# Optimization experiments

Hardware: AMD Instinct MI355X
Metric: run time of the kernel (lower is better)

Reference implementation:

```python
import jax, jax.numpy as jnp
import numpy as np

B, IMG, TXT = 1, 2048, 256
D_MODEL = 2048
HEADS, HEAD_DIM = 16, 128
INNER = HEADS * HEAD_DIM
EPS = 1e-5
SCALE = HEAD_DIM ** -0.5


def _rmsnorm(x, w):
    # normalize over last dim (head_dim)
    return (x * jax.lax.rsqrt(jnp.mean(x * x, axis=-1, keepdims=True) + EPS)) * w


def _rope(x, cos, sin):
    # x: (B, S, H, D); cos/sin: (S, D) with pairwise-repeated freqs (interleaved convention)
    c = cos[None, :, None, :]
    s = sin[None, :, None, :]
    x1 = x[..., 0::2]
    x2 = x[..., 1::2]
    rot = jnp.stack([-x2, x1], axis=-1).reshape(x.shape)
    return x * c + rot * s


def setup_inputs() -> dict:
    key = jax.random.key(0)
    ks = jax.random.split(key, 12)
    sc_in = D_MODEL ** -0.5
    sc_inner = INNER ** -0.5
    inp = {
        'hidden_states': jax.random.normal(ks[0], (B, IMG, D_MODEL), jnp.float32),
        'encoder_hidden_states': jax.random.normal(ks[1], (B, TXT, D_MODEL), jnp.float32),
    }
    # RoPE tables over the joint (text + image) sequence, interleaved pair layout
    pos = jnp.arange(TXT + IMG, dtype=jnp.float32)
    inv = 1.0 / (10000.0 ** (jnp.arange(0, HEAD_DIM, 2, dtype=jnp.float32) / HEAD_DIM))
    freqs = pos[:, None] * inv[None, :]
    freqs = jnp.repeat(freqs, 2, axis=-1)  # (S, HEAD_DIM)
    inp['freqs_cos'] = jnp.cos(freqs)
    inp['freqs_sin'] = jnp.sin(freqs)
    # parameters (stored (in, out))
    inp['Wqkv'] = jax.random.normal(ks[2], (D_MODEL, 3 * INNER), jnp.float32) * sc_in
    inp['Wqkv_add'] = jax.random.normal(ks[3], (D_MODEL, 3 * INNER), jnp.float32) * sc_in
    inp['b_qkv_add'] = jax.random.normal(ks[4], (3 * INNER,), jnp.float32) * 0.01
    inp['norm_q_w'] = jnp.ones((HEAD_DIM,), jnp.float32)
    inp['norm_k_w'] = jnp.ones((HEAD_DIM,), jnp.float32)
    inp['norm_aq_w'] = jnp.ones((HEAD_DIM,), jnp.float32)
    inp['norm_ak_w'] = jnp.ones((HEAD_DIM,), jnp.float32)
    inp['Wout'] = jax.random.normal(ks[5], (INNER, D_MODEL), jnp.float32) * sc_inner
    inp['b_out'] = jax.random.normal(ks[6], (D_MODEL,), jnp.float32) * 0.01
    inp['Wadd_out'] = jax.random.normal(ks[7], (INNER, D_MODEL), jnp.float32) * sc_inner
    inp['b_add_out'] = jax.random.normal(ks[8], (D_MODEL,), jnp.float32) * 0.01
    return inp


def reference(hidden_states, encoder_hidden_states, freqs_cos, freqs_sin,
              Wqkv, Wqkv_add, b_qkv_add, norm_q_w, norm_k_w, norm_aq_w, norm_ak_w,
              Wout, b_out, Wadd_out, b_add_out):
    b, s_img, _ = hidden_states.shape
    s_txt = encoder_hidden_states.shape[1]

    # fused QKV projection (image stream), chunk q/k/v, unflatten heads
    qkv = hidden_states @ Wqkv  # (B, IMG, 3*INNER)
    q, k, v = jnp.split(qkv, 3, axis=-1)
    q = _rmsnorm(q.reshape(b, s_img, HEADS, HEAD_DIM), norm_q_w)
    k = _rmsnorm(k.reshape(b, s_img, HEADS, HEAD_DIM), norm_k_w)
    v = v.reshape(b, s_img, HEADS, HEAD_DIM)

    # fused QKV projection (text stream, with bias)
    eqkv = encoder_hidden_states @ Wqkv_add + b_qkv_add
    eq, ek, ev = jnp.split(eqkv, 3, axis=-1)
    eq = _rmsnorm(eq.reshape(b, s_txt, HEADS, HEAD_DIM), norm_aq_w)
    ek = _rmsnorm(ek.reshape(b, s_txt, HEADS, HEAD_DIM), norm_ak_w)
    ev = ev.reshape(b, s_txt, HEADS, HEAD_DIM)

    # joint [text; image] concatenation, then RoPE on joint Q/K
    jq = jnp.concatenate([eq, q], axis=1)
    jk = jnp.concatenate([ek, k], axis=1)
    jv = jnp.concatenate([ev, v], axis=1)
    jq = _rope(jq, freqs_cos, freqs_sin)
    jk = _rope(jk, freqs_cos, freqs_sin)

    # non-causal scaled dot-product attention, layout (B, S, H, D)
    scores = jnp.einsum('bqhd,bkhd->bhqk', jq, jk) * SCALE
    probs = jax.nn.softmax(scores, axis=-1)
    out = jnp.einsum('bhqk,bkhd->bqhd', probs, jv)  # (B, S_joint, H, D)
    out = out.reshape(b, s_txt + s_img, INNER)

    enc_out = out[:, :s_txt]
    img_out = out[:, s_txt:]
    img_out = img_out @ Wout + b_out
    enc_out = enc_out @ Wadd_out + b_add_out
    return (img_out, enc_out)
```

## Files before the change

kernel.cpp:

```cpp
#include <hip/hip_runtime.h>
#include <stdint.h>

#define HEADS 16
#define HD 128
#define S_TXT 256
#define S_IMG 2048
#define S_ALL 2304
#define DMODEL 2048
#define N_QKV 6144
#define INNER 2048
#define ATT_EPS 1e-5f
#define ATT_SCALE 0.08838834764831845f
#define LOG2E 1.4426950408889634f
#define MBOUND 16.5f
#define QT_N 18
#define TPS 36

typedef __attribute__((ext_vector_type(8))) __bf16 bf16x8;
typedef __attribute__((ext_vector_type(4))) float f32x4;
typedef __attribute__((ext_vector_type(4))) uint32_t u32x4;

__device__ __forceinline__ uint16_t f2bf(float f) {
  union { float f; uint32_t u; } v; v.f = f;
  uint32_t r = (v.u + 0x7FFF + ((v.u >> 16) & 1)) >> 16;
  return (uint16_t)r;
}
__device__ __forceinline__ float bf2f(uint16_t h) {
  union { float f; uint32_t u; } v; v.u = ((uint32_t)h) << 16;
  return v.f;
}
__device__ __forceinline__ float fexp2(float x) {
#if __has_builtin(__builtin_amdgcn_exp2f)
  return __builtin_amdgcn_exp2f(x);
#else
  return __expf(x * 0.69314718055994531f);
#endif
}

__device__ __forceinline__ void async_cp16(const void* g, void* l) {
  __builtin_amdgcn_global_load_lds(
      (const __attribute__((address_space(1))) void*)g,
      (__attribute__((address_space(3))) void*)l, 16, 0, 0);
}

__global__ __launch_bounds__(256) void k_cvt(const float* __restrict__ src,
                                             uint16_t* __restrict__ dst, int n4) {
  int i = blockIdx.x * 256 + threadIdx.x;
  int stride = gridDim.x * 256;
  for (; i < n4; i += stride) {
    float4 v = ((const float4*)src)[i];
    uint16_t o[4];
    o[0] = f2bf(v.x); o[1] = f2bf(v.y); o[2] = f2bf(v.z); o[3] = f2bf(v.w);
    ((uint2*)dst)[i] = *(const uint2*)o;
  }
}

__global__ __launch_bounds__(256) void k_cvt_t4(
    const float* __restrict__ s0, uint16_t* __restrict__ d0,
    const float* __restrict__ s1, uint16_t* __restrict__ d1,
    const float* __restrict__ s2, uint16_t* __restrict__ d2,
    const float* __restrict__ s3, uint16_t* __restrict__ d3) {
  __shared__ float t[64][68];
  int b = blockIdx.x;
  const float* src; uint16_t* dst; int R, C, tb;
  if (b < 3072)      { src = s0; dst = d0; R = DMODEL; C = N_QKV;  tb = b; }
  else if (b < 6144) { src = s1; dst = d1; R = DMODEL; C = N_QKV;  tb = b - 3072; }
  else if (b < 7168) { src = s2; dst = d2; R = INNER;  C = DMODEL; tb = b - 6144; }
  else               { src = s3; dst = d3; R = INNER;  C = DMODEL; tb = b - 7168; }
  int ntr = R >> 6;
  int tr = tb % ntr, tc = tb / ntr;
  int tid = threadIdx.x;
  int rr = tid >> 4, c4 = (tid & 15) * 4;
#pragma unroll
  for (int j = 0; j < 4; ++j) {
    int r = rr + j * 16;
    float4 v = *(const float4*)&src[(size_t)(tr * 64 + r) * C + tc * 64 + c4];
    *(float4*)&t[r][c4] = v;
  }
  __syncthreads();
  int cc = tid >> 4, r4 = (tid & 15) * 4;
#pragma unroll
  for (int j = 0; j < 4; ++j) {
    int c = cc + j * 16;
    uint16_t ov[4];
    ov[0] = f2bf(t[r4 + 0][c]); ov[1] = f2bf(t[r4 + 1][c]);
    ov[2] = f2bf(t[r4 + 2][c]); ov[3] = f2bf(t[r4 + 3][c]);
    *(uint2*)&dst[(size_t)(tc * 64 + c) * R + tr * 64 + r4] = *(const uint2*)ov;
  }
}

template <bool OUT_BF16>
__global__ __launch_bounds__(512, 1) void k_gemm2(
    const uint16_t* __restrict__ A0, const uint16_t* __restrict__ B0,
    const float* __restrict__ bias0, void* __restrict__ C0,
    const uint16_t* __restrict__ A1, const uint16_t* __restrict__ B1,
    const float* __restrict__ bias1, void* __restrict__ C1,
    int seg0_tiles, int N, int K) {
  __shared__ __align__(16) char lds[3 * 49152];
  int bn = blockIdx.x, bm = blockIdx.y;
  const uint16_t* A; const uint16_t* B; const float* bias; void* C; int mrow;
  if (bm < seg0_tiles) { A = A0; B = B0; bias = bias0; C = C0; mrow = bm * 256; }
  else { A = A1; B = B1; bias = bias1; C = C1; mrow = (bm - seg0_tiles) * 256; }
  int tid = threadIdx.x, lane = tid & 63, w = tid >> 6;
  int g = lane >> 4, li = lane & 15;
  int wm = w >> 1, wn = w & 1;
  const int NKI = K / 64;

  int rowin = lane >> 3;
  int csrc = (lane & 7) ^ rowin;

  auto stage = [&](int t, char* buf) {
    int kt = t * 64;
#pragma unroll
    for (int j = 0; j < 4; ++j) {
      int r = w * 4 + j;
      int tr = r * 8 + rowin;
      async_cp16(A + (size_t)(mrow + tr) * K + kt + 8 * csrc, buf + r * 1024);
    }
#pragma unroll
    for (int j = 0; j < 2; ++j) {
      int r = w * 2 + j;
      int tr = r * 8 + rowin;
      async_cp16(B + (size_t)(bn * 128 + tr) * K + kt + 8 * csrc, buf + 32768 + r * 1024);
    }
  };

  f32x4 acc[4][4] = {};

  stage(0, lds);
  stage(1, lds + 49152);
  asm volatile("s_waitcnt vmcnt(6)" ::: "memory");
  __builtin_amdgcn_s_barrier();
  asm volatile("" ::: "memory");

  int cbuf = 0, sbuf = 2;
  for (int t = 0; t < NKI; ++t) {
    const char* cur = lds + cbuf * 49152;
    if (t + 2 < NKI) stage(t + 2, lds + sbuf * 49152);

    bf16x8 af[2][4], bfv[2][4];
#pragma unroll
    for (int kk = 0; kk < 2; ++kk) {
#pragma unroll
      for (int mi = 0; mi < 4; ++mi) {
        int row = wm * 64 + mi * 16 + li;
        int ch = (kk * 4 + g) ^ (row & 7);
        af[kk][mi] = __builtin_bit_cast(bf16x8, *(const u32x4*)(cur + row * 128 + ch * 16));
      }
#pragma unroll
      for (int ni = 0; ni < 4; ++ni) {
        int row = wn * 64 + ni * 16 + li;
        int ch = (kk * 4 + g) ^ (row & 7);
        bfv[kk][ni] = __builtin_bit_cast(bf16x8, *(const u32x4*)(cur + 32768 + row * 128 + ch * 16));
      }
    }
    __builtin_amdgcn_s_setprio(1);
#pragma unroll
    for (int kk = 0; kk < 2; ++kk)
#pragma unroll
      for (int mi = 0; mi < 4; ++mi)
#pragma unroll
        for (int ni = 0; ni < 4; ++ni)
          acc[mi][ni] = __builtin_amdgcn_mfma_f32_16x16x32_bf16(af[kk][mi], bfv[kk][ni], acc[mi][ni], 0, 0, 0);
    __builtin_amdgcn_s_setprio(0);

    if (t + 1 < NKI) {
      if (t + 2 < NKI) asm volatile("s_waitcnt vmcnt(6)" ::: "memory");
      else             asm volatile("s_waitcnt vmcnt(0)" ::: "memory");
      __builtin_amdgcn_s_barrier();
      asm volatile("" ::: "memory");
    }
    cbuf = (cbuf + 1 == 3) ? 0 : cbuf + 1;
    sbuf = (sbuf + 1 == 3) ? 0 : sbuf + 1;
  }

#pragma unroll
  for (int mi = 0; mi < 4; ++mi) {
#pragma unroll
    for (int ni = 0; ni < 4; ++ni) {
      int col = bn * 128 + wn * 64 + ni * 16 + li;
      float bv = bias ? bias[col] : 0.0f;
#pragma unroll
      for (int i = 0; i < 4; ++i) {
        int r = mrow + wm * 64 + mi * 16 + 4 * g + i;
        float v = acc[mi][ni][i] + bv;
        if (OUT_BF16) ((uint16_t*)C)[(size_t)r * N + col] = f2bf(v);
        else          ((float*)C)[(size_t)r * N + col] = v;
      }
    }
  }
}

__global__ __launch_bounds__(256) void k_post(
    const uint16_t* __restrict__ qkv_img, const uint16_t* __restrict__ qkv_txt,
    const float* __restrict__ fcos, const float* __restrict__ fsin,
    const float* __restrict__ wq, const float* __restrict__ wk,
    const float* __restrict__ waq, const float* __restrict__ wak,
    uint16_t* __restrict__ Qo, uint16_t* __restrict__ Ko, uint16_t* __restrict__ VTo) {
  int s = blockIdx.x;
  const uint16_t* row = (s < S_TXT) ? qkv_txt + (size_t)s * N_QKV
                                    : qkv_img + (size_t)(s - S_TXT) * N_QKV;
  const float* wqp = (s < S_TXT) ? waq : wq;
  const float* wkp = (s < S_TXT) ? wak : wk;
  int tid = threadIdx.x, lane = tid & 63, w = tid >> 6;
  int h = w * 4 + (lane >> 4);
  int d0 = (lane & 15) * 8;
  float cs[8], sn[8];
#pragma unroll
  for (int j = 0; j < 8; ++j) {
    cs[j] = fcos[s * HD + d0 + j];
    sn[j] = fsin[s * HD + d0 + j];
  }
#pragma unroll
  for (int part = 0; part < 2; ++part) {
    const uint16_t* src = row + part * INNER + h * HD + d0;
    u32x4 raw = *(const u32x4*)src;
    const uint16_t* rp = (const uint16_t*)&raw;
    float x[8], ss = 0.f;
#pragma unroll
    for (int j = 0; j < 8; ++j) { x[j] = bf2f(rp[j]); ss += x[j] * x[j]; }
    ss += __shfl_xor(ss, 1); ss += __shfl_xor(ss, 2);
    ss += __shfl_xor(ss, 4); ss += __shfl_xor(ss, 8);
    float rn = rsqrtf(ss * (1.0f / HD) + ATT_EPS);
    const float* wp = part ? wkp : wqp;
#pragma unroll
    for (int j = 0; j < 8; ++j) x[j] = x[j] * rn * wp[d0 + j];
    float y[8];
#pragma unroll
    for (int j = 0; j < 8; j += 2) {
      y[j]     = x[j] * cs[j] - x[j + 1] * sn[j];
      y[j + 1] = x[j + 1] * cs[j + 1] + x[j] * sn[j + 1];
    }
    float sc = part ? 1.0f : (ATT_SCALE * LOG2E);
    uint16_t ov[8];
#pragma unroll
    for (int j = 0; j < 8; ++j) ov[j] = f2bf(y[j] * sc);
    uint16_t* dst = (part ? Ko : Qo) + ((size_t)h * S_ALL + s) * HD + d0;
    *(u32x4*)dst = *(const u32x4*)ov;
  }
  {
    u32x4 raw = *(const u32x4*)(row + 2 * INNER + h * HD + d0);
    const uint16_t* rp = (const uint16_t*)&raw;
#pragma unroll
    for (int j = 0; j < 8; ++j)
      VTo[((size_t)h * HD + d0 + j) * S_ALL + s] = rp[j];
  }
}

__global__ __launch_bounds__(256, 3) void k_attn(
    const uint16_t* __restrict__ Qg, const uint16_t* __restrict__ Kg,
    const uint16_t* __restrict__ VTg,
    float* __restrict__ part0, float* __restrict__ part1,
    float* __restrict__ lsumP) {
  __shared__ __align__(16) char Kt[2][8192];
  __shared__ __align__(16) char Vt[2][8192];
  __shared__ __align__(16) uint16_t Pl[4][32 * 40];

  int b0 = blockIdx.x;
  int bid = (b0 & 7) * 72 + (b0 >> 3);
  int h = bid / 36, r6 = bid % 36, sp = r6 / 18, qt = r6 % 18;
  int tid = threadIdx.x, lane = tid & 63, w = tid >> 6;
  int g = lane >> 4, li = lane & 15;

  const uint16_t* Kh = Kg + (size_t)h * S_ALL * HD;
  const uint16_t* Vh = VTg + (size_t)h * HD * S_ALL;
  float* po = (sp ? part1 : part0) + ((size_t)(h * QT_N + qt) * 128 + w * 32) * 128;

  int qbase = qt * 128 + w * 32;
  bf16x8 qf[2][4];
#pragma unroll
  for (int q2 = 0; q2 < 2; ++q2) {
    const uint16_t* qp = Qg + ((size_t)h * S_ALL + qbase + q2 * 16 + li) * HD;
#pragma unroll
    for (int kc = 0; kc < 4; ++kc)
      qf[q2][kc] = __builtin_bit_cast(bf16x8, *(const u32x4*)(qp + kc * 32 + g * 8));
  }
  f32x4 o[2][8] = {};
  float lsum[2] = {0.f, 0.f};

  auto stage = [&](int tk, int buf) {
#pragma unroll
    for (int j = 0; j < 2; ++j) {
      int cj = w * 128 + j * 64 + lane;
      int row = cj >> 4, c = (cj & 15) ^ (row & 15);
      async_cp16(Kh + (size_t)(tk * 32 + row) * HD + 8 * c, Kt[buf] + (w * 128 + j * 64) * 16);
    }
#pragma unroll
    for (int j = 0; j < 2; ++j) {
      int cj = w * 128 + j * 64 + lane;
      int row = cj >> 2, c = (cj & 3) ^ ((row >> 1) & 3);
      async_cp16(Vh + (size_t)row * S_ALL + tk * 32 + 8 * c, Vt[buf] + (w * 128 + j * 64) * 16);
    }
  };

  int t0 = sp * TPS;
  stage(t0, 0);
  asm volatile("s_waitcnt vmcnt(0)" ::: "memory");
  __builtin_amdgcn_s_barrier();
  asm volatile("" ::: "memory");

  for (int t = 0; t < TPS; ++t) {
    int cur = t & 1;
    if (t + 1 < TPS) stage(t0 + t + 1, cur ^ 1);
    const char* KtC = Kt[cur];
    const char* VtC = Vt[cur];

    f32x4 sc[2][2];
#pragma unroll
    for (int q2 = 0; q2 < 2; ++q2)
#pragma unroll
      for (int kb = 0; kb < 2; ++kb)
        sc[q2][kb] = (f32x4){-MBOUND, -MBOUND, -MBOUND, -MBOUND};
    __builtin_amdgcn_s_setprio(1);
#pragma unroll
    for (int kb = 0; kb < 2; ++kb)
#pragma unroll
      for (int kc = 0; kc < 4; ++kc) {
        int ch = (kc * 4 + g) ^ li;
        bf16x8 kf = __builtin_bit_cast(bf16x8,
            *(const u32x4*)(KtC + (kb * 16 + li) * 256 + ch * 16));
        sc[0][kb] = __builtin_amdgcn_mfma_f32_16x16x32_bf16(kf, qf[0][kc], sc[0][kb], 0, 0, 0);
        sc[1][kb] = __builtin_amdgcn_mfma_f32_16x16x32_bf16(kf, qf[1][kc], sc[1][kb], 0, 0, 0);
      }
    __builtin_amdgcn_s_setprio(0);

    uint16_t* Pw = &Pl[w][0];
#pragma unroll
    for (int q2 = 0; q2 < 2; ++q2)
#pragma unroll
      for (int kb = 0; kb < 2; ++kb) {
        float p0 = fexp2(sc[q2][kb][0]);
        float p1 = fexp2(sc[q2][kb][1]);
        float p2 = fexp2(sc[q2][kb][2]);
        float p3 = fexp2(sc[q2][kb][3]);
        lsum[q2] += (p0 + p1) + (p2 + p3);
        uint2 pk;
        pk.x = (uint32_t)f2bf(p0) | ((uint32_t)f2bf(p1) << 16);
        pk.y = (uint32_t)f2bf(p2) | ((uint32_t)f2bf(p3) << 16);
        *(uint2*)((char*)Pw + (q2 * 16 + li) * 80 + kb * 32 + g * 8) = pk;
      }

    bf16x8 pf[2];
#pragma unroll
    for (int q2 = 0; q2 < 2; ++q2)
      pf[q2] = __builtin_bit_cast(bf16x8,
          *(const u32x4*)((const char*)Pw + (q2 * 16 + li) * 80 + g * 16));
    __builtin_amdgcn_s_setprio(1);
#pragma unroll
    for (int db = 0; db < 8; ++db) {
      int vrow = db * 16 + li;
      int ch = g ^ ((vrow >> 1) & 3);
      bf16x8 vf = __builtin_bit_cast(bf16x8, *(const u32x4*)(VtC + vrow * 64 + ch * 16));
      o[0][db] = __builtin_amdgcn_mfma_f32_16x16x32_bf16(pf[0], vf, o[0][db], 0, 0, 0);
      o[1][db] = __builtin_amdgcn_mfma_f32_16x16x32_bf16(pf[1], vf, o[1][db], 0, 0, 0);
    }
    __builtin_amdgcn_s_setprio(0);

    asm volatile("s_waitcnt vmcnt(0)" ::: "memory");
    __builtin_amdgcn_s_barrier();
    asm volatile("" ::: "memory");
  }

#pragma unroll
  for (int q2 = 0; q2 < 2; ++q2) {
    float v = lsum[q2];
    v += __shfl_xor(v, 16);
    v += __shfl_xor(v, 32);
    lsum[q2] = v;
  }
  if (lane < 16) {
#pragma unroll
    for (int q2 = 0; q2 < 2; ++q2)
      lsumP[((size_t)sp * HEADS + h) * S_ALL + qbase + q2 * 16 + lane] = lsum[q2];
  }
#pragma unroll
  for (int q2 = 0; q2 < 2; ++q2)
#pragma unroll
    for (int db = 0; db < 8; ++db)
#pragma unroll
      for (int i = 0; i < 4; ++i)
        po[(q2 * 16 + 4 * g + i) * 128 + db * 16 + li] = o[q2][db][i];
}

__global__ __launch_bounds__(256) void k_comb(
    const float* __restrict__ p0, const float* __restrict__ p1,
    const float* __restrict__ lsumP, uint16_t* __restrict__ attn) {
  int q = blockIdx.x, qt = q >> 7, ql = q & 127;
#pragma unroll
  for (int rep = 0; rep < 2; ++rep) {
    int d4 = threadIdx.x + rep * 256;
    int d = d4 * 4, h = d >> 7, dl = d & 127;
    size_t off = (((size_t)h * QT_N + qt) * 128 + ql) * 128 + dl;
    float4 a = *(const float4*)&p0[off];
    float4 b = *(const float4*)&p1[off];
    float l0 = lsumP[(size_t)h * S_ALL + q];
    float l1 = lsumP[((size_t)HEADS + h) * S_ALL + q];
    float inv = 1.0f / (l0 + l1);
    uint16_t ov[4];
    ov[0] = f2bf((a.x + b.x) * inv); ov[1] = f2bf((a.y + b.y) * inv);
    ov[2] = f2bf((a.z + b.z) * inv); ov[3] = f2bf((a.w + b.w) * inv);
    *(uint2*)&attn[(size_t)q * INNER + d] = *(const uint2*)ov;
  }
}

extern "C" void kernel_launch(void* const* d_in, const int* in_sizes, int n_in,
                              void* d_out, int out_size, void* d_ws, size_t ws_size,
                              hipStream_t stream) {
  const float* hidden = (const float*)d_in[0];
  const float* enc    = (const float*)d_in[1];
  const float* fcos   = (const float*)d_in[2];
  const float* fsin   = (const float*)d_in[3];
  const float* Wqkv   = (const float*)d_in[4];
  const float* Wqkva  = (const float*)d_in[5];
  const float* bqkva  = (const float*)d_in[6];
  const float* nqw    = (const float*)d_in[7];
  const float* nkw    = (const float*)d_in[8];
  const float* naqw   = (const float*)d_in[9];
  const float* nakw   = (const float*)d_in[10];
  const float* Wout   = (const float*)d_in[11];
  const float* bout   = (const float*)d_in[12];
  const float* Wadd   = (const float*)d_in[13];
  const float* badd   = (const float*)d_in[14];
  float* out_img = (float*)d_out;
  float* out_enc = (float*)d_out + (size_t)S_IMG * DMODEL;

  char* ws = (char*)d_ws;
  size_t off = 0;
  auto alloc = [&](size_t bytes) {
    char* p = ws + off;
    off += (bytes + 255) & ~(size_t)255;
    return p;
  };
  uint16_t* hs_bf   = (uint16_t*)alloc((size_t)S_IMG * DMODEL * 2);
  uint16_t* enc_bf  = (uint16_t*)alloc((size_t)S_TXT * DMODEL * 2);
  char*     wqkv_base = alloc((size_t)N_QKV * DMODEL * 2 * 2);
  uint16_t* WqkvT   = (uint16_t*)wqkv_base;
  uint16_t* WqkvaT  = (uint16_t*)(wqkv_base + (size_t)N_QKV * DMODEL * 2);
  uint16_t* WoutT   = (uint16_t*)alloc((size_t)DMODEL * INNER * 2);
  uint16_t* WaddT   = (uint16_t*)alloc((size_t)DMODEL * INNER * 2);
  uint16_t* qkv_img = (uint16_t*)alloc((size_t)S_IMG * N_QKV * 2);
  uint16_t* qkv_txt = (uint16_t*)alloc((size_t)S_TXT * N_QKV * 2);
  uint16_t* Qb   = (uint16_t*)wqkv_base;
  uint16_t* Kb   = Qb + (size_t)HEADS * S_ALL * HD;
  uint16_t* VTb  = Kb + (size_t)HEADS * S_ALL * HD;
  uint16_t* attn = VTb + (size_t)HEADS * S_ALL * HD;
  float* part0 = (float*)d_out;
  float* part1 = (float*)qkv_img;
  float* lsumP = (float*)enc_bf;

  k_cvt<<<1024, 256, 0, stream>>>(hidden, hs_bf, S_IMG * DMODEL / 4);
  k_cvt<<<256, 256, 0, stream>>>(enc, enc_bf, S_TXT * DMODEL / 4);
  k_cvt_t4<<<8192, 256, 0, stream>>>(Wqkv, WqkvT, Wqkva, WqkvaT, Wout, WoutT, Wadd, WaddT);

  dim3 gq(N_QKV / 128, (S_TXT + S_IMG) / 256);
  k_gemm2<true><<<gq, 512, 0, stream>>>(enc_bf, WqkvaT, bqkva, qkv_txt,
                                        hs_bf, WqkvT, nullptr, qkv_img,
                                        1, N_QKV, DMODEL);

  k_post<<<S_ALL, 256, 0, stream>>>(qkv_img, qkv_txt, fcos, fsin,
                                    nqw, nkw, naqw, nakw, Qb, Kb, VTb);

  k_attn<<<HEADS * QT_N * 2, 256, 0, stream>>>(Qb, Kb, VTb, part0, part1, lsumP);
  k_comb<<<S_ALL, 256, 0, stream>>>(part0, part1, lsumP, attn);

  dim3 go(DMODEL / 128, S_ALL / 256);
  k_gemm2<false><<<go, 512, 0, stream>>>(attn, WaddT, badd, out_enc,
                                         attn + (size_t)S_TXT * INNER, WoutT, bout, out_img,
                                         1, DMODEL, DMODEL);
}
```

Before: 252.1 us.

## Interleave QKV GEMM loads with MFMA phases and add smaller-tile output GEMM

The QKV GEMM k-loop is split into four phases. Each phase issues part of the next stage's async copies, loads fragments for half the N sub-tiles, and runs MFMAs between barriers, so global copies, LDS reads and matrix math overlap at finer grain. The output projection moves to a new 128x128-tile, 256-thread kernel with 32-wide K double buffering and up to four blocks per CU. That raises the block count for the 2304x2048 output GEMM (288 vs 144 tiles) to fill more CUs. The cost is many extra barriers per iteration in the QKV GEMM and less data reuse per block in the output GEMM.

```diff
diff --git a/kernel.cpp b/kernel.cpp
--- a/kernel.cpp
+++ b/kernel.cpp
@@ -89,16 +89,15 @@
   }
 }
 
-template <bool OUT_BF16>
 __global__ __launch_bounds__(512, 1) void k_gemm2(
     const uint16_t* __restrict__ A0, const uint16_t* __restrict__ B0,
-    const float* __restrict__ bias0, void* __restrict__ C0,
+    const float* __restrict__ bias0, uint16_t* __restrict__ C0,
     const uint16_t* __restrict__ A1, const uint16_t* __restrict__ B1,
-    const float* __restrict__ bias1, void* __restrict__ C1,
+    const float* __restrict__ bias1, uint16_t* __restrict__ C1,
     int seg0_tiles, int N, int K) {
   __shared__ __align__(16) char lds[3 * 49152];
   int bn = blockIdx.x, bm = blockIdx.y;
-  const uint16_t* A; const uint16_t* B; const float* bias; void* C; int mrow;
+  const uint16_t* A; const uint16_t* B; const float* bias; uint16_t* C; int mrow;
   if (bm < seg0_tiles) { A = A0; B = B0; bias = bias0; C = C0; mrow = bm * 256; }
   else { A = A1; B = B1; bias = bias1; C = C1; mrow = (bm - seg0_tiles) * 256; }
   int tid = threadIdx.x, lane = tid & 63, w = tid >> 6;
@@ -109,14 +108,17 @@
   int rowin = lane >> 3;
   int csrc = (lane & 7) ^ rowin;
 
-  auto stage = [&](int t, char* buf) {
+  auto stage_a = [&](int t, char* buf, int j0) {
     int kt = t * 64;
 #pragma unroll
-    for (int j = 0; j < 4; ++j) {
+    for (int j = j0; j < j0 + 2; ++j) {
       int r = w * 4 + j;
       int tr = r * 8 + rowin;
       async_cp16(A + (size_t)(mrow + tr) * K + kt + 8 * csrc, buf + r * 1024);
     }
+  };
+  auto stage_b = [&](int t, char* buf) {
+    int kt = t * 64;
 #pragma unroll
     for (int j = 0; j < 2; ++j) {
       int r = w * 2 + j;
@@ -127,8 +129,8 @@
 
   f32x4 acc[4][4] = {};
 
-  stage(0, lds);
-  stage(1, lds + 49152);
+  stage_a(0, lds, 0); stage_a(0, lds, 2); stage_b(0, lds);
+  stage_a(1, lds + 49152, 0); stage_a(1, lds + 49152, 2); stage_b(1, lds + 49152);
   asm volatile("s_waitcnt vmcnt(6)" ::: "memory");
   __builtin_amdgcn_s_barrier();
   asm volatile("" ::: "memory");
@@ -136,40 +138,88 @@
   int cbuf = 0, sbuf = 2;
   for (int t = 0; t < NKI; ++t) {
     const char* cur = lds + cbuf * 49152;
-    if (t + 2 < NKI) stage(t + 2, lds + sbuf * 49152);
-
-    bf16x8 af[2][4], bfv[2][4];
-#pragma unroll
-    for (int kk = 0; kk < 2; ++kk) {
-#pragma unroll
-      for (int mi = 0; mi < 4; ++mi) {
-        int row = wm * 64 + mi * 16 + li;
-        int ch = (kk * 4 + g) ^ (row & 7);
-        af[kk][mi] = __builtin_bit_cast(bf16x8, *(const u32x4*)(cur + row * 128 + ch * 16));
-      }
-#pragma unroll
-      for (int ni = 0; ni < 4; ++ni) {
-        int row = wn * 64 + ni * 16 + li;
-        int ch = (kk * 4 + g) ^ (row & 7);
-        bfv[kk][ni] = __builtin_bit_cast(bf16x8, *(const u32x4*)(cur + 32768 + row * 128 + ch * 16));
-      }
-    }
+    char* stg = lds + sbuf * 49152;
+    bool pre = (t + 2 < NKI);
+
+    bf16x8 af[4], bfv[2];
+    if (pre) stage_a(t + 2, stg, 0);
+#pragma unroll
+    for (int mi = 0; mi < 4; ++mi) {
+      int row = wm * 64 + mi * 16 + li;
+      af[mi] = __builtin_bit_cast(bf16x8, *(const u32x4*)(cur + row * 128 + (g ^ (row & 7)) * 16));
+    }
+#pragma unroll
+    for (int ni = 0; ni < 2; ++ni) {
+      int row = wn * 64 + ni * 16 + li;
+      bfv[ni] = __builtin_bit_cast(bf16x8, *(const u32x4*)(cur + 32768 + row * 128 + (g ^ (row & 7)) * 16));
+    }
+    __builtin_amdgcn_s_barrier();
     __builtin_amdgcn_s_setprio(1);
 #pragma unroll
-    for (int kk = 0; kk < 2; ++kk)
-#pragma unroll
-      for (int mi = 0; mi < 4; ++mi)
-#pragma unroll
-        for (int ni = 0; ni < 4; ++ni)
-          acc[mi][ni] = __builtin_amdgcn_mfma_f32_16x16x32_bf16(af[kk][mi], bfv[kk][ni], acc[mi][ni], 0, 0, 0);
+    for (int mi = 0; mi < 4; ++mi)
+#pragma unroll
+      for (int ni = 0; ni < 2; ++ni)
+        acc[mi][ni] = __builtin_amdgcn_mfma_f32_16x16x32_bf16(af[mi], bfv[ni], acc[mi][ni], 0, 0, 0);
     __builtin_amdgcn_s_setprio(0);
+    __builtin_amdgcn_s_barrier();
+
+    if (pre) stage_a(t + 2, stg, 2);
+#pragma unroll
+    for (int ni = 0; ni < 2; ++ni) {
+      int row = wn * 64 + (ni + 2) * 16 + li;
+      bfv[ni] = __builtin_bit_cast(bf16x8, *(const u32x4*)(cur + 32768 + row * 128 + (g ^ (row & 7)) * 16));
+    }
+    __builtin_amdgcn_s_barrier();
+    __builtin_amdgcn_s_setprio(1);
+#pragma unroll
+    for (int mi = 0; mi < 4; ++mi)
+#pragma unroll
+      for (int ni = 0; ni < 2; ++ni)
+        acc[mi][ni + 2] = __builtin_amdgcn_mfma_f32_16x16x32_bf16(af[mi], bfv[ni], acc[mi][ni + 2], 0, 0, 0);
+    __builtin_amdgcn_s_setprio(0);
+    __builtin_amdgcn_s_barrier();
+
+    if (pre) stage_b(t + 2, stg);
+#pragma unroll
+    for (int mi = 0; mi < 4; ++mi) {
+      int row = wm * 64 + mi * 16 + li;
+      af[mi] = __builtin_bit_cast(bf16x8, *(const u32x4*)(cur + row * 128 + ((4 + g) ^ (row & 7)) * 16));
+    }
+#pragma unroll
+    for (int ni = 0; ni < 2; ++ni) {
+      int row = wn * 64 + ni * 16 + li;
+      bfv[ni] = __builtin_bit_cast(bf16x8, *(const u32x4*)(cur + 32768 + row * 128 + ((4 + g) ^ (row & 7)) * 16));
+    }
+    __builtin_amdgcn_s_barrier();
+    __builtin_amdgcn_s_setprio(1);
+#pragma unroll
+    for (int mi = 0; mi < 4; ++mi)
+#pragma unroll
+      for (int ni = 0; ni < 2; ++ni)
+        acc[mi][ni] = __builtin_amdgcn_mfma_f32_16x16x32_bf16(af[mi], bfv[ni], acc[mi][ni], 0, 0, 0);
+    __builtin_amdgcn_s_setprio(0);
+    __builtin_amdgcn_s_barrier();
+
+#pragma unroll
+    for (int ni = 0; ni < 2; ++ni) {
+      int row = wn * 64 + (ni + 2) * 16 + li;
+      bfv[ni] = __builtin_bit_cast(bf16x8, *(const u32x4*)(cur + 32768 + row * 128 + ((4 + g) ^ (row & 7)) * 16));
+    }
+    __builtin_amdgcn_s_barrier();
+    __builtin_amdgcn_s_setprio(1);
+#pragma unroll
+    for (int mi = 0; mi < 4; ++mi)
+#pragma unroll
+      for (int ni = 0; ni < 2; ++ni)
+        acc[mi][ni + 2] = __builtin_amdgcn_mfma_f32_16x16x32_bf16(af[mi], bfv[ni], acc[mi][ni + 2], 0, 0, 0);
+    __builtin_amdgcn_s_setprio(0);
 
     if (t + 1 < NKI) {
-      if (t + 2 < NKI) asm volatile("s_waitcnt vmcnt(6)" ::: "memory");
-      else             asm volatile("s_waitcnt vmcnt(0)" ::: "memory");
-      __builtin_amdgcn_s_barrier();
-      asm volatile("" ::: "memory");
-    }
+      if (pre) asm volatile("s_waitcnt vmcnt(6)" ::: "memory");
+      else     asm volatile("s_waitcnt vmcnt(0)" ::: "memory");
+    }
+    __builtin_amdgcn_s_barrier();
+    asm volatile("" ::: "memory");
     cbuf = (cbuf + 1 == 3) ? 0 : cbuf + 1;
     sbuf = (sbuf + 1 == 3) ? 0 : sbuf + 1;
   }
@@ -183,9 +233,94 @@
 #pragma unroll
       for (int i = 0; i < 4; ++i) {
         int r = mrow + wm * 64 + mi * 16 + 4 * g + i;
-        float v = acc[mi][ni][i] + bv;
-        if (OUT_BF16) ((uint16_t*)C)[(size_t)r * N + col] = f2bf(v);
-        else          ((float*)C)[(size_t)r * N + col] = v;
+        C[(size_t)r * N + col] = f2bf(acc[mi][ni][i] + bv);
+      }
+    }
+  }
+}
+
+__global__ __launch_bounds__(256, 4) void k_gemmO(
+    const uint16_t* __restrict__ A0, const uint16_t* __restrict__ B0,
+    const float* __restrict__ bias0, float* __restrict__ C0,
+    const uint16_t* __restrict__ A1, const uint16_t* __restrict__ B1,
+    const float* __restrict__ bias1, float* __restrict__ C1,
+    int seg0_tiles, int N, int K) {
+  __shared__ __align__(16) char lds[4 * 8192];
+  int bn = blockIdx.x, bm = blockIdx.y;
+  const uint16_t* A; const uint16_t* B; const float* bias; float* C; int mrow;
+  if (bm < seg0_tiles) { A = A0; B = B0; bias = bias0; C = C0; mrow = bm * 128; }
+  else { A = A1; B = B1; bias = bias1; C = C1; mrow = (bm - seg0_tiles) * 128; }
+  int tid = threadIdx.x, lane = tid & 63, w = tid >> 6;
+  int g = lane >> 4, li = lane & 15;
+  int wm = w >> 1, wn = w & 1;
+  const int NKT = K / 32;
+
+  int rowin = lane >> 2;
+  int csrc = (lane & 3) ^ (rowin & 3);
+
+  auto stage = [&](int t, int buf) {
+    int kt = t * 32;
+#pragma unroll
+    for (int j = 0; j < 2; ++j) {
+      int r = w * 2 + j;
+      int tr = r * 16 + rowin;
+      async_cp16(A + (size_t)(mrow + tr) * K + kt + 8 * csrc, lds + buf * 8192 + r * 1024);
+    }
+#pragma unroll
+    for (int j = 0; j < 2; ++j) {
+      int r = w * 2 + j;
+      int tr = r * 16 + rowin;
+      async_cp16(B + (size_t)(bn * 128 + tr) * K + kt + 8 * csrc, lds + 16384 + buf * 8192 + r * 1024);
+    }
+  };
+
+  f32x4 acc[4][4] = {};
+  stage(0, 0);
+  asm volatile("s_waitcnt vmcnt(0)" ::: "memory");
+  __builtin_amdgcn_s_barrier();
+  asm volatile("" ::: "memory");
+
+  for (int t = 0; t < NKT; ++t) {
+    int cur = t & 1;
+    bool pre = (t + 1 < NKT);
+    if (pre) stage(t + 1, cur ^ 1);
+    const char* Ac = lds + cur * 8192;
+    const char* Bc = lds + 16384 + cur * 8192;
+
+    bf16x8 af[4], bfv[4];
+#pragma unroll
+    for (int mi = 0; mi < 4; ++mi) {
+      int row = wm * 64 + mi * 16 + li;
+      af[mi] = __builtin_bit_cast(bf16x8, *(const u32x4*)(Ac + row * 64 + (g ^ (row & 3)) * 16));
+    }
+#pragma unroll
+    for (int ni = 0; ni < 4; ++ni) {
+      int row = wn * 64 + ni * 16 + li;
+      bfv[ni] = __builtin_bit_cast(bf16x8, *(const u32x4*)(Bc + row * 64 + (g ^ (row & 3)) * 16));
+    }
+    __builtin_amdgcn_s_setprio(1);
+#pragma unroll
+    for (int mi = 0; mi < 4; ++mi)
+#pragma unroll
+      for (int ni = 0; ni < 4; ++ni)
+        acc[mi][ni] = __builtin_amdgcn_mfma_f32_16x16x32_bf16(af[mi], bfv[ni], acc[mi][ni], 0, 0, 0);
+    __builtin_amdgcn_s_setprio(0);
+
+    if (pre) asm volatile("s_waitcnt vmcnt(0)" ::: "memory");
+    __builtin_amdgcn_s_barrier();
+    asm volatile("" ::: "memory");
+  }
+
+#pragma unroll
+  for (int mi = 0; mi < 4; ++mi) {
+#pragma unroll
+    for (int ni = 0; ni < 4; ++ni) {
+      int col = bn * 128 + wn * 64 + ni * 16 + li;
+      float bv = bias[col];
+#pragma unroll
+      for (int i = 0; i < 4; ++i) {
+        int r = mrow + wm * 64 + mi * 16 + 4 * g + i;
+        C[(size_t)r * N + col] = acc[mi][ni][i] + bv;
       }
     }
   }
@@ -453,9 +588,9 @@
   k_cvt_t4<<<8192, 256, 0, stream>>>(Wqkv, WqkvT, Wqkva, WqkvaT, Wout, WoutT, Wadd, WaddT);
 
   dim3 gq(N_QKV / 128, (S_TXT + S_IMG) / 256);
-  k_gemm2<true><<<gq, 512, 0, stream>>>(enc_bf, WqkvaT, bqkva, qkv_txt,
-                                        hs_bf, WqkvT, nullptr, qkv_img,
-                                        1, N_QKV, DMODEL);
+  k_gemm2<<<gq, 512, 0, stream>>>(enc_bf, WqkvaT, bqkva, qkv_txt,
+                                  hs_bf, WqkvT, nullptr, qkv_img,
+                                  1, N_QKV, DMODEL);
 
   k_post<<<S_ALL, 256, 0, stream>>>(qkv_img, qkv_txt, fcos, fsin,
                                     nqw, nkw, naqw, nakw, Qb, Kb, VTb);
@@ -463,8 +598,8 @@
   k_attn<<<HEADS * QT_N * 2, 256, 0, stream>>>(Qb, Kb, VTb, part0, part1, lsumP);
   k_comb<<<S_ALL, 256, 0, stream>>>(part0, part1, lsumP, attn);
 
-  dim3 go(DMODEL / 128, S_ALL / 256);
-  k_gemm2<false><<<go, 512, 0, stream>>>(attn, WaddT, badd, out_enc,
-                                         attn + (size_t)S_TXT * INNER, WoutT, bout, out_img,
-                                         1, DMODEL, DMODEL);
-}
+  dim3 go(DMODEL / 128, S_ALL / 128);
+  k_gemmO<<<go, 256, 0, stream>>>(attn, WaddT, badd, out_enc,
+                                  attn + (size_t)S_TXT * INNER, WoutT, bout, out_img,
+                                  2, DMODEL, DMODEL);
+}
```

Result: slower. 258.8 us (+2.6%).
